# Optimization experiments

Measured on AMD Instinct MI355X. Metric: run time of the kernel, lower is better.

Reference implementation:

```python
import jax, jax.numpy as jnp
import numpy as np

B, L, D, H = 1, 4096, 768, 12
HD = D // H  # 64
NEG_INF = jnp.finfo(jnp.float32).min


def rmsnorm(x, g, eps=1e-6):
    return x * jax.lax.rsqrt(jnp.mean(x * x, axis=-1, keepdims=True) + eps) * g


def activation_quant(x):
    # per-token 8-bit fake quant
    scale = 127.0 / jnp.clip(jnp.max(jnp.abs(x), axis=-1, keepdims=True), 1e-5)
    return jnp.clip(jnp.round(x * scale), -128, 127) / scale


def weight_quant(w):
    # per-tensor 1.58-bit (ternary) fake quant
    scale = 1.0 / jnp.clip(jnp.mean(jnp.abs(w)), 1e-5)
    return jnp.clip(jnp.round(w * scale), -1, 1) / scale


def bitlinear(x, w, g):
    xn = rmsnorm(x, g)
    xq = xn + jax.lax.stop_gradient(activation_quant(xn) - xn)  # STE
    wq = w + jax.lax.stop_gradient(weight_quant(w) - w)          # STE
    return xq @ wq.T


def rope(x, cos, sin):
    # x: [B,L,H,HD]; cos/sin: [L,HD/2] -> broadcast [1,L,1,HD/2]
    xr = x.reshape(*x.shape[:-1], HD // 2, 2)
    x0, x1 = xr[..., 0], xr[..., 1]
    c = cos[None, :, None, :]
    s = sin[None, :, None, :]
    o0 = x0 * c - x1 * s
    o1 = x0 * s + x1 * c
    return jnp.stack([o0, o1], axis=-1).reshape(x.shape)


def setup_inputs() -> dict:
    key = jax.random.key(0)
    k1, k2, k3 = jax.random.split(key, 3)
    hidden_states = jax.random.normal(k1, (B, L, D), dtype=jnp.float32)
    mask = jnp.ones((B, L), dtype=bool)
    # standard RoPE angles, theta=10000
    freqs = 1.0 / (10000.0 ** (np.arange(0, HD, 2, dtype=np.float32) / HD))
    ang = np.outer(np.arange(L, dtype=np.float32), freqs)
    rot_cos = jnp.asarray(np.cos(ang), dtype=jnp.float32)
    rot_sin = jnp.asarray(np.sin(ang), dtype=jnp.float32)
    w_qkv = jax.random.truncated_normal(k2, -2.0, 2.0, (3 * D, D), dtype=jnp.float32) * 0.002
    w_o = jax.random.truncated_normal(k3, -2.0, 2.0, (D, D), dtype=jnp.float32) * 0.002
    g_qkv_norm = jnp.ones((D,), dtype=jnp.float32)
    g_o_norm = jnp.ones((D,), dtype=jnp.float32)
    return {"hidden_states": hidden_states, "mask": mask, "rot_cos": rot_cos,
            "rot_sin": rot_sin, "w_qkv": w_qkv, "w_o": w_o,
            "g_qkv_norm": g_qkv_norm, "g_o_norm": g_o_norm}


def reference(hidden_states, mask, rot_cos, rot_sin, w_qkv, w_o, g_qkv_norm, g_o_norm):
    qkv = bitlinear(hidden_states, w_qkv, g_qkv_norm)        # [B,L,3D]
    xq, xk, xv = jnp.split(qkv, 3, axis=-1)
    xq = xq.reshape(B, L, H, HD)
    xk = xk.reshape(B, L, H, HD)
    xv = xv.reshape(B, L, H, HD)
    xq = rope(xq, rot_cos, rot_sin)
    xk = rope(xk, rot_cos, rot_sin)
    scale = 1.0 / jnp.sqrt(jnp.float32(HD))
    scores = jnp.einsum('blhd,bmhd->bhlm', xq, xk) * scale   # [B,H,L,L]
    bias = jnp.where(mask[:, None, :, None], 0.0, NEG_INF)   # [B,1,L,1]
    attn = jax.nn.softmax(scores + bias, axis=-1)
    out = jnp.einsum('bhlm,bmhd->blhd', attn, xv).reshape(B, L, D)
    return bitlinear(out, w_o, g_o_norm)                      # dropout_p = 0.0
```

## Files before the change

### kernel.cpp

```cpp
#include <hip/hip_runtime.h>
#include <hip/hip_bf16.h>
#include <cstdint>
#include <cstddef>

typedef __attribute__((ext_vector_type(8))) short short8;
typedef __attribute__((ext_vector_type(4))) float f32x4;
typedef __attribute__((ext_vector_type(4))) int i32x4;
typedef unsigned short u16;
typedef unsigned int u32;
typedef signed char i8s;

#define DEV __device__ __forceinline__

DEV float bf2f(u16 u){ union{unsigned int i; float f;} v; v.i=((unsigned int)u)<<16; return v.f; }
DEV u16 f2bf(float x){ union{float f; unsigned int i;} v; v.f=x; unsigned int b=v.i; return (u16)((b + 0x7FFFu + ((b>>16)&1u))>>16); }
DEV u32 packbf2(float lo, float hi){
  __hip_bfloat162 h2 = __float22bfloat162_rn(float2{lo, hi});
  union{ __hip_bfloat162 h; u32 u; } cv; cv.h = h2; return cv.u;
}
DEV u32 pack4i8(float a, float b, float c, float d){
  int ia=(int)a, ib=(int)b, ic=(int)c, id=(int)d;
  return (u32)(ia & 0xff) | (((u32)(ib & 0xff))<<8) | (((u32)(ic & 0xff))<<16) | (((u32)(id & 0xff))<<24);
}
DEV void gll16(const void* gsrc, void* lds){
  __builtin_amdgcn_global_load_lds((const __attribute__((address_space(1))) unsigned int*)gsrc,
                                   (__attribute__((address_space(3))) unsigned int*)lds, 16, 0, 0);
}

__global__ __launch_bounds__(256) void prelude(
    const float* __restrict__ wa, int na, const float* __restrict__ wb, int nb,
    float* __restrict__ pa, float* __restrict__ pb,
    const float* __restrict__ x, const float* __restrict__ g,
    i8s* __restrict__ xq, float* __restrict__ deq)
{
  if(blockIdx.x < 512){
    __shared__ float red[256];
    const bool second = blockIdx.x >= 256;
    const float4* w4 = (const float4*)(second ? wb : wa);
    const int n4     = (second ? nb : na) >> 2;
    float* part      = second ? pb : pa;
    const int b0     = second ? (int)blockIdx.x - 256 : (int)blockIdx.x;
    float s=0.f;
    for(int i=b0*256+threadIdx.x; i<n4; i+=256*256){
      float4 v = w4[i];
      s += (fabsf(v.x)+fabsf(v.y)) + (fabsf(v.z)+fabsf(v.w));
    }
    red[threadIdx.x]=s; __syncthreads();
    for(int st=128; st>0; st>>=1){ if(threadIdx.x<st) red[threadIdx.x]+=red[threadIdx.x+st]; __syncthreads(); }
    if(threadIdx.x==0) part[b0]=red[0];
  } else {
    const int t = threadIdx.x, lane = t&63, w = t>>6;
    const int row = ((int)blockIdx.x - 512)*4 + w;
    const float* xr = x + (size_t)row*768;
    float4 v[3], gg[3];
#pragma unroll
    for(int j=0;j<3;j++){
      v[j]  = *(const float4*)(xr + lane*4 + j*256);
      gg[j] = *(const float4*)(g  + lane*4 + j*256);
    }
    float ss = 0.f;
#pragma unroll
    for(int j=0;j<3;j++) ss += v[j].x*v[j].x + v[j].y*v[j].y + v[j].z*v[j].z + v[j].w*v[j].w;
#pragma unroll
    for(int d=1; d<64; d<<=1) ss += __shfl_xor(ss, d, 64);
    float rn = rsqrtf(ss*(1.0f/768.f) + 1e-6f);
    float n[12];
#pragma unroll
    for(int j=0;j<3;j++){
      n[j*4+0]=v[j].x*rn*gg[j].x; n[j*4+1]=v[j].y*rn*gg[j].y;
      n[j*4+2]=v[j].z*rn*gg[j].z; n[j*4+3]=v[j].w*rn*gg[j].w;
    }
    float am = 0.f;
#pragma unroll
    for(int e=0;e<12;e++) am = fmaxf(am, fabsf(n[e]));
#pragma unroll
    for(int d=1; d<64; d<<=1) am = fmaxf(am, __shfl_xor(am, d, 64));
    float mx = fmaxf(am, 1e-5f);
    float sc = 127.f/mx;
    i8s* o = xq + (size_t)row*768;
#pragma unroll
    for(int j=0;j<3;j++){
      float q0 = fminf(127.f, fmaxf(-128.f, rintf(n[j*4+0]*sc)));
      float q1 = fminf(127.f, fmaxf(-128.f, rintf(n[j*4+1]*sc)));
      float q2 = fminf(127.f, fmaxf(-128.f, rintf(n[j*4+2]*sc)));
      float q3 = fminf(127.f, fmaxf(-128.f, rintf(n[j*4+3]*sc)));
      *(u32*)(o + lane*4 + j*256) = pack4i8(q0,q1,q2,q3);
    }
    if(lane==0) deq[row]=mx*(1.0f/127.f);
  }
}

__global__ void quant_weight2(const float* __restrict__ wa, int na, const float* __restrict__ pa_, float inva, float* __restrict__ sa, i8s* __restrict__ qa,
                              const float* __restrict__ wb, int nb, const float* __restrict__ pb_, float invb, float* __restrict__ sb, i8s* __restrict__ qb){
  __shared__ float red[256];
  const bool second = blockIdx.x >= 1024;
  const float* part = second ? pb_ : pa_;
  red[threadIdx.x] = part[threadIdx.x]; __syncthreads();
  for(int st=128; st>0; st>>=1){ if(threadIdx.x<st) red[threadIdx.x]+=red[threadIdx.x+st]; __syncthreads(); }
  float scale = fmaxf(red[0]*(second?invb:inva), 1e-5f);
  const float4* w4 = (const float4*)(second ? wb : wa);
  i8s* q           = second ? qb : qa;
  const int n4     = (second ? nb : na) >> 2;
  const int b0     = second ? (int)blockIdx.x - 1024 : (int)blockIdx.x;
  const int nblk   = second ? 512 : 1024;
  if(threadIdx.x==0 && b0==0) (second?sb:sa)[0] = scale;
  float inv = 1.0f/scale;
  for(int i=b0*256+threadIdx.x; i<n4; i+=nblk*256){
    float4 v = w4[i];
    float q0 = fminf(1.f,fmaxf(-1.f,rintf(v.x*inv)));
    float q1 = fminf(1.f,fmaxf(-1.f,rintf(v.y*inv)));
    float q2 = fminf(1.f,fmaxf(-1.f,rintf(v.z*inv)));
    float q3 = fminf(1.f,fmaxf(-1.f,rintf(v.w*inv)));
    *(u32*)(q + (size_t)i*4) = pack4i8(q0,q1,q2,q3);
  }
}

__global__ __launch_bounds__(256) void rms_quant(const float* __restrict__ x, const float* __restrict__ g,
                          i8s* __restrict__ xq, float* __restrict__ deq){
  const int t = threadIdx.x, lane = t&63, w = t>>6;
  const int row = blockIdx.x*4 + w;
  const float* xr = x + (size_t)row*768;
  float4 v[3], gg[3];
#pragma unroll
  for(int j=0;j<3;j++){
    v[j]  = *(const float4*)(xr + lane*4 + j*256);
    gg[j] = *(const float4*)(g  + lane*4 + j*256);
  }
  float ss = 0.f;
#pragma unroll
  for(int j=0;j<3;j++) ss += v[j].x*v[j].x + v[j].y*v[j].y + v[j].z*v[j].z + v[j].w*v[j].w;
#pragma unroll
  for(int d=1; d<64; d<<=1) ss += __shfl_xor(ss, d, 64);
  float rn = rsqrtf(ss*(1.0f/768.f) + 1e-6f);
  float n[12];
#pragma unroll
  for(int j=0;j<3;j++){
    n[j*4+0]=v[j].x*rn*gg[j].x; n[j*4+1]=v[j].y*rn*gg[j].y;
    n[j*4+2]=v[j].z*rn*gg[j].z; n[j*4+3]=v[j].w*rn*gg[j].w;
  }
  float am = 0.f;
#pragma unroll
  for(int e=0;e<12;e++) am = fmaxf(am, fabsf(n[e]));
#pragma unroll
  for(int d=1; d<64; d<<=1) am = fmaxf(am, __shfl_xor(am, d, 64));
  float mx = fmaxf(am, 1e-5f);
  float sc = 127.f/mx;
  i8s* o = xq + (size_t)row*768;
#pragma unroll
  for(int j=0;j<3;j++){
    float q0 = fminf(127.f, fmaxf(-128.f, rintf(n[j*4+0]*sc)));
    float q1 = fminf(127.f, fmaxf(-128.f, rintf(n[j*4+1]*sc)));
    float q2 = fminf(127.f, fmaxf(-128.f, rintf(n[j*4+2]*sc)));
    float q3 = fminf(127.f, fmaxf(-128.f, rintf(n[j*4+3]*sc)));
    *(u32*)(o + lane*4 + j*256) = pack4i8(q0,q1,q2,q3);
  }
  if(lane==0) deq[row]=mx*(1.0f/127.f);
}

template<int BM, int BN>
__global__ __launch_bounds__(256) void gemm_i8(
    const i8s* __restrict__ A, const i8s* __restrict__ B,
    int M, int N, int K,
    const float* __restrict__ rdeq, const float* __restrict__ wsc,
    u16* __restrict__ Cb, float* __restrict__ Cf)
{
  constexpr int MR = BM/32, NR = BN/32;
  constexpr int SA = BM/64, SB = BN/64;
  __shared__ i8s lA[3][4][BM][16];
  __shared__ i8s lB[3][4][BN][16];
  const int t = threadIdx.x, lane = t&63, w = t>>6;
  const int wr = (w>>1)*(BM/2), wc = (w&1)*(BN/2);
  const int rowBase = blockIdx.y*BM, colBase = blockIdx.x*BN;
  const int g = lane>>4, lr = lane&15;
  i32x4 acc[MR][NR];
#pragma unroll
  for(int m=0;m<MR;m++)
#pragma unroll
    for(int n=0;n<NR;n++) acc[m][n]={0,0,0,0};

  auto stage = [&](int p, int k0){
#pragma unroll
    for(int i=0;i<SA;i++){
      int s = t + i*256, r = s & (BM-1), kg = s / BM;
      gll16(A + (size_t)(rowBase+r)*K + k0 + kg*16, &lA[p][kg][r][0]);
    }
#pragma unroll
    for(int i=0;i<SB;i++){
      int s = t + i*256, r = s & (BN-1), kg = s / BN;
      gll16(B + (size_t)(colBase+r)*K + k0 + kg*16, &lB[p][kg][r][0]);
    }
  };

  const int nk = K>>6;
  stage(0, 0);
  if(nk>1) stage(1, 64);
  int p = 0;
  for(int kt=0; kt<nk; ++kt){
    if(kt+2<nk) stage((p+2)%3, (kt+2)<<6);
    if constexpr (SA+SB == 4){
      if(kt+2<nk)      asm volatile("s_waitcnt vmcnt(8)" ::: "memory");
      else if(kt+1<nk) asm volatile("s_waitcnt vmcnt(4)" ::: "memory");
      else             asm volatile("s_waitcnt vmcnt(0)" ::: "memory");
    } else {
      if(kt+2<nk)      asm volatile("s_waitcnt vmcnt(4)" ::: "memory");
      else if(kt+1<nk) asm volatile("s_waitcnt vmcnt(2)" ::: "memory");
      else             asm volatile("s_waitcnt vmcnt(0)" ::: "memory");
    }
    __builtin_amdgcn_s_barrier();
    __builtin_amdgcn_sched_barrier(0);
    i32x4 af[MR], bfr[NR];
#pragma unroll
    for(int m=0;m<MR;m++) af[m]  = *(const i32x4*)&lA[p][g][wr + m*16 + lr][0];
#pragma unroll
    for(int n=0;n<NR;n++) bfr[n] = *(const i32x4*)&lB[p][g][wc + n*16 + lr][0];
#pragma unroll
    for(int m=0;m<MR;m++)
#pragma unroll
      for(int n=0;n<NR;n++)
        acc[m][n] = __builtin_amdgcn_mfma_i32_16x16x64_i8(af[m], bfr[n], acc[m][n], 0,0,0);
    __builtin_amdgcn_s_barrier();
    p = (p+1)%3;
  }
  float ws = wsc[0];
#pragma unroll
  for(int m=0;m<MR;m++){
#pragma unroll
    for(int rr=0;rr<4;rr++){
      int row = rowBase + wr + m*16 + g*4 + rr;
      float rs = rdeq[row]*ws;
#pragma unroll
      for(int n=0;n<NR;n++){
        int col = colBase + wc + n*16 + lr;
        float v = (float)acc[m][n][rr]*rs;
        if(Cb) Cb[(size_t)row*N+col]=f2bf(v);
        else   Cf[(size_t)row*N+col]=v;
      }
    }
  }
}

__global__ __launch_bounds__(256) void rope_split(const u16* __restrict__ qkv,
                           const float* __restrict__ cosb, const float* __restrict__ sinb,
                           u16* __restrict__ Qb, u16* __restrict__ Kb, u16* __restrict__ Vt)
{
  const float SC = 0.125f*1.44269504088896f;
  const int h = blockIdx.y, p0 = blockIdx.x*64, t = threadIdx.x;
#pragma unroll
  for(int it=0; it<8; ++it){
    int idx = it*256 + t;
    int pos = p0 + (idx>>5), j = idx&31;
    const u16* base = qkv + (size_t)pos*2304 + h*64;
    float q0=bf2f(base[2*j]), q1=bf2f(base[2*j+1]);
    float k0=bf2f(base[768+2*j]), k1=bf2f(base[768+2*j+1]);
    float c=cosb[pos*32+j], s=sinb[pos*32+j];
    size_t ob = ((size_t)h*4096 + pos)*64 + 2*j;
    Qb[ob]   = f2bf((q0*c - q1*s)*SC);
    Qb[ob+1] = f2bf((q0*s + q1*c)*SC);
    Kb[ob]   = f2bf(k0*c - k1*s);
    Kb[ob+1] = f2bf(k0*s + k1*c);
  }
  __shared__ u16 vt[64][72];
#pragma unroll
  for(int it=0; it<2; ++it){
    int idx = it*256 + t;
    int pos = idx>>3, db = idx&7;
    uint4 v = *(const uint4*)(qkv + (size_t)(p0+pos)*2304 + h*64 + 1536 + db*8);
    const u16* pv = (const u16*)&v;
#pragma unroll
    for(int e=0;e<8;e++) vt[db*8+e][pos] = pv[e];
  }
  __syncthreads();
#pragma unroll
  for(int it=0; it<2; ++it){
    int idx = it*256 + t;
    int d = idx>>3, pc = idx&7;
    uint4 tmp; u16* tp=(u16*)&tmp;
#pragma unroll
    for(int e=0;e<8;e++) tp[e]=vt[d][pc*8+e];
    *(uint4*)(Vt + ((size_t)h*64 + d)*4096 + p0 + pc*8) = tmp;
  }
}

__global__ __launch_bounds__(256) void attn(
    const u16* __restrict__ Qb, const u16* __restrict__ Kb,
    const u16* __restrict__ Vt, float* __restrict__ O)
{
  __shared__ u16 lK[8][128][8];
  __shared__ u16 lV[16][64][8];
  __shared__ u32 lPT[4][16][64];

  const int bid = blockIdx.x;
  const int swz = (bid&7)*96 + (bid>>3);
  const int h = swz>>6, q0 = (swz&63)*64;
  const int t = threadIdx.x, lane = t&63, w = t>>6;
  const int g = lane>>4, lr = lane&15;
  const int key = (lr<<2)&28;

  short8 qf0, qf1;
  {
    const u16* qp = Qb + ((size_t)h*4096 + q0 + w*16 + lr)*64 + g*8;
    qf0 = *(const short8*)qp;
    qf1 = *(const short8*)(qp+32);
  }
  f32x4 o[4];
#pragma unroll
  for(int n=0;n<4;n++) o[n]={0.f,0.f,0.f,0.f};
  f32x4 l4 = {0.f,0.f,0.f,0.f};

  const u16* kb_lane = Kb + ((size_t)h*4096 + lane)*64;
  const u16* vb_lane = Vt + ((size_t)h*64  + lane)*4096;
  const int kvhalf = (w&1)*64;

  for(int it=0; it<32; ++it){
    const int kvb = it<<7;
    __syncthreads();
#pragma unroll
    for(int j=0;j<4;j++){
      int sl = j*4 + w;
      gll16(kb_lane + (size_t)(kvb + kvhalf)*64 + (sl>>1)*8, &lK[sl>>1][kvhalf][0]);
    }
#pragma unroll
    for(int j=0;j<4;j++){
      int sl = j*4 + w;
      gll16(vb_lane + kvb + sl*8, &lV[sl][0][0]);
    }
    __syncthreads();

    f32x4 s[8];
    __builtin_amdgcn_s_setprio(1);
#pragma unroll
    for(int nt=0;nt<8;nt++){
      f32x4 z = {0.f,0.f,0.f,0.f};
      short8 kf0 = *(const short8*)&lK[g  ][nt*16+lr][0];
      short8 kf1 = *(const short8*)&lK[g+4][nt*16+lr][0];
      z = __builtin_amdgcn_mfma_f32_16x16x32_bf16(kf0, qf0, z, 0,0,0);
      s[nt] = __builtin_amdgcn_mfma_f32_16x16x32_bf16(kf1, qf1, z, 0,0,0);
    }
    __builtin_amdgcn_s_setprio(0);

#pragma unroll
    for(int nt=0;nt<8;nt++){
      float p0 = __builtin_amdgcn_exp2f(s[nt][0]);
      float p1 = __builtin_amdgcn_exp2f(s[nt][1]);
      float p2 = __builtin_amdgcn_exp2f(s[nt][2]);
      float p3 = __builtin_amdgcn_exp2f(s[nt][3]);
      l4 += (f32x4){p0,p1,p2,p3};
      uint2 pk; pk.x = packbf2(p0,p1); pk.y = packbf2(p2,p3);
      *(uint2*)&lPT[w][lr][(nt*8 + g*2) ^ key] = pk;
    }

#pragma unroll
    for(int c=0;c<4;c++){
      short8 pa = *(const short8*)&lPT[w][lr][(c*16 + g*4) ^ key];
#pragma unroll
      for(int nt=0;nt<4;nt++){
        short8 vf = *(const short8*)&lV[c*4+g][nt*16+lr][0];
        o[nt] = __builtin_amdgcn_mfma_f32_16x16x32_bf16(pa, vf, o[nt], 0,0,0);
      }
    }
  }
  float l_run = (l4[0]+l4[1])+(l4[2]+l4[3]);
  l_run += __shfl_xor(l_run, 16, 64);
  l_run += __shfl_xor(l_run, 32, 64);
  float linv[4];
#pragma unroll
  for(int r=0;r<4;r++) linv[r] = 1.0f/__shfl(l_run, g*4+r, 64);
#pragma unroll
  for(int nt=0;nt<4;nt++)
#pragma unroll
    for(int r=0;r<4;r++){
      int row = q0 + w*16 + g*4 + r;
      O[(size_t)row*768 + h*64 + nt*16 + lr] = o[nt][r]*linv[r];
    }
}

extern "C" void kernel_launch(void* const* d_in, const int* in_sizes, int n_in,
                              void* d_out, int out_size, void* d_ws, size_t ws_size,
                              hipStream_t stream) {
  const float* hidden = (const float*)d_in[0];
  (void)d_in[1];
  const float* cosb = (const float*)d_in[2];
  const float* sinb = (const float*)d_in[3];
  const float* w_qkv = (const float*)d_in[4];
  const float* w_o   = (const float*)d_in[5];
  const float* g_qkv = (const float*)d_in[6];
  const float* g_o   = (const float*)d_in[7];
  float* out = (float*)d_out;
  (void)in_sizes; (void)n_in; (void)out_size;

  uint8_t* ws = (uint8_t*)d_ws;
  size_t off = 0;
  auto alloc = [&](size_t bytes)->size_t{ size_t o=off; off=(off+bytes+255)&~(size_t)255; return o; };
  size_t o_sc0  = alloc(4);
  size_t o_sc1  = alloc(4);
  size_t o_pt0  = alloc(256*4);
  size_t o_pt1  = alloc(256*4);
  size_t o_adeq = alloc(4096*4);
  size_t o_odeq = alloc(4096*4);
  size_t o_wq   = alloc((size_t)2304*768);
  size_t o_wo   = alloc((size_t)768*768);
  size_t o_xq   = alloc((size_t)4096*768);
  size_t o_qkv  = alloc((size_t)4096*2304*2);
  size_t o_q    = alloc((size_t)12*4096*64*2);
  size_t o_k    = alloc((size_t)12*4096*64*2);
  size_t o_vt   = alloc((size_t)12*64*4096*2);
  size_t o_of   = alloc((size_t)4096*768*4);
  size_t o_oq   = alloc((size_t)4096*768);
  if (off > ws_size) {
    hipMemsetAsync(d_out, 0, (size_t)out_size*4, stream);
    return;
  }
  float* sc0 = (float*)(ws+o_sc0); float* sc1 = (float*)(ws+o_sc1);
  float* pt0 = (float*)(ws+o_pt0); float* pt1 = (float*)(ws+o_pt1);
  float* adeq= (float*)(ws+o_adeq); float* odeq=(float*)(ws+o_odeq);
  i8s* Wq  = (i8s*)(ws+o_wq);  i8s* Wo  = (i8s*)(ws+o_wo);
  i8s* Xq  = (i8s*)(ws+o_xq);  u16* QKV = (u16*)(ws+o_qkv);
  u16* Qb  = (u16*)(ws+o_q);   u16* Kb  = (u16*)(ws+o_k);
  u16* Vt  = (u16*)(ws+o_vt);
  float* Of = (float*)(ws+o_of); i8s* Oq = (i8s*)(ws+o_oq);

  prelude<<<1536,256,0,stream>>>(w_qkv, 2304*768, w_o, 768*768, pt0, pt1,
                                 hidden, g_qkv, Xq, adeq);
  quant_weight2<<<1536,256,0,stream>>>(w_qkv, 2304*768, pt0, 1.0f/(2304.f*768.f), sc0, Wq,
                                       w_o,   768*768,  pt1, 1.0f/(768.f*768.f),  sc1, Wo);
  gemm_i8<128,128><<<dim3(18,32),256,0,stream>>>(Xq, Wq, 4096,2304,768, adeq, sc0, QKV, nullptr);
  rope_split<<<dim3(64,12),256,0,stream>>>(QKV, cosb, sinb, Qb, Kb, Vt);
  attn<<<768,256,0,stream>>>(Qb, Kb, Vt, Of);
  rms_quant<<<1024,256,0,stream>>>(Of, g_o, Oq, odeq);
  gemm_i8<64,64><<<dim3(12,64),256,0,stream>>>(Oq, Wo, 4096,768,768, odeq, sc1, nullptr, out);
}
```

Before: 157.9 us.

## Double-buffer K/V LDS tiles to overlap global loads with attention compute

Splits the K and V shared-memory tiles into two buffers and issues the global-to-LDS loads for the next KV block before computing the current one. A manual vmcnt wait plus a raw barrier replaces the two __syncthreads per iteration. This hides load latency behind the MFMA work, at the cost of doubling LDS use for K/V, which may lower occupancy. Correctness depends on the vmcnt(8) count matching the eight outstanding loads per thread and on LDS visibility across waves without an lgkmcnt wait.

```diff
diff --git a/kernel.cpp b/kernel.cpp
--- a/kernel.cpp
+++ b/kernel.cpp
@@ -285,8 +285,8 @@
     const u16* __restrict__ Qb, const u16* __restrict__ Kb,
     const u16* __restrict__ Vt, float* __restrict__ O)
 {
-  __shared__ u16 lK[8][128][8];
-  __shared__ u16 lV[16][64][8];
+  __shared__ u16 lK[2][8][128][8];
+  __shared__ u16 lV[2][16][64][8];
   __shared__ u32 lPT[4][16][64];
 
   const int bid = blockIdx.x;
@@ -311,28 +311,38 @@
   const u16* vb_lane = Vt + ((size_t)h*64  + lane)*4096;
   const int kvhalf = (w&1)*64;
 
-  for(int it=0; it<32; ++it){
-    const int kvb = it<<7;
-    __syncthreads();
+  auto stage = [&](int p, int kvb){
 #pragma unroll
     for(int j=0;j<4;j++){
       int sl = j*4 + w;
-      gll16(kb_lane + (size_t)(kvb + kvhalf)*64 + (sl>>1)*8, &lK[sl>>1][kvhalf][0]);
+      gll16(kb_lane + (size_t)(kvb + kvhalf)*64 + (sl>>1)*8, &lK[p][sl>>1][kvhalf][0]);
     }
 #pragma unroll
     for(int j=0;j<4;j++){
       int sl = j*4 + w;
-      gll16(vb_lane + kvb + sl*8, &lV[sl][0][0]);
-    }
-    __syncthreads();
+      gll16(vb_lane + kvb + sl*8, &lV[p][sl][0][0]);
+    }
+  };
+
+  stage(0, 0);
+  for(int it=0; it<32; ++it){
+    const int p = it&1;
+    if(it+1<32){
+      stage(p^1, (it+1)<<7);
+      asm volatile("s_waitcnt vmcnt(8)" ::: "memory");
+    } else {
+      asm volatile("s_waitcnt vmcnt(0)" ::: "memory");
+    }
+    __builtin_amdgcn_s_barrier();
+    __builtin_amdgcn_sched_barrier(0);
 
     f32x4 s[8];
     __builtin_amdgcn_s_setprio(1);
 #pragma unroll
     for(int nt=0;nt<8;nt++){
       f32x4 z = {0.f,0.f,0.f,0.f};
-      short8 kf0 = *(const short8*)&lK[g  ][nt*16+lr][0];
-      short8 kf1 = *(const short8*)&lK[g+4][nt*16+lr][0];
+      short8 kf0 = *(const short8*)&lK[p][g  ][nt*16+lr][0];
+      short8 kf1 = *(const short8*)&lK[p][g+4][nt*16+lr][0];
       z = __builtin_amdgcn_mfma_f32_16x16x32_bf16(kf0, qf0, z, 0,0,0);
       s[nt] = __builtin_amdgcn_mfma_f32_16x16x32_bf16(kf1, qf1, z, 0,0,0);
     }
@@ -354,10 +364,11 @@
       short8 pa = *(const short8*)&lPT[w][lr][(c*16 + g*4) ^ key];
 #pragma unroll
       for(int nt=0;nt<4;nt++){
-        short8 vf = *(const short8*)&lV[c*4+g][nt*16+lr][0];
+        short8 vf = *(const short8*)&lV[p][c*4+g][nt*16+lr][0];
         o[nt] = __builtin_amdgcn_mfma_f32_16x16x32_bf16(pa, vf, o[nt], 0,0,0);
       }
     }
+    __builtin_amdgcn_s_barrier();
   }
   float l_run = (l4[0]+l4[1])+(l4[2]+l4[3]);
   l_run += __shfl_xor(l_run, 16, 64);
```

Result: slower. 200.1 us (+26.7%).
